# Kernel tuning notes

Measured on AMD Instinct MI355X. Metric: run time of the kernel, lower is better.

## Reference

```python
import jax, jax.numpy as jnp
import numpy as np

EPS = 1e-12  # torch F.normalize eps
NEG = -9999.0  # masked_fill value from the source


def _l2norm(x):
    n = jnp.linalg.norm(x, axis=-1, keepdims=True)
    return x / jnp.maximum(n, EPS)


def _maxsim(q, d, mask_f, mask_b):
    # q: [B,Lq,D]; d: [N,B,Ld,D]; mask: [N,B,Ld]
    rep = _l2norm(d * mask_f[..., None])
    s = jnp.einsum('bqd,nbkd->nbqk', q, rep)  # [N,B,Lq,Ld]
    s = jnp.where(mask_b[:, :, None, :], s, NEG)
    return s.max(axis=-1).sum(axis=-1)  # [N,B]


def setup_inputs() -> dict:
    key = jax.random.key(0)
    k0, k1, k2, k3, k4 = jax.random.split(key, 5)
    B, N, Lq, Ld, D = 128, 8, 32, 256, 128
    return {
        'q_reps': jax.random.normal(k0, (B, Lq, D), jnp.float32),
        'd_cq': jax.random.normal(k1, (N, B, Ld, D), jnp.float32),
        'd_orig': jax.random.normal(k2, (N, B, Ld, D), jnp.float32),
        'd_mask': jax.random.randint(k3, (N, B, Ld), 0, 2).astype(jnp.int32),
        'labels': jax.random.normal(k4, (B, N), jnp.float32),
    }


def reference(q_reps, d_cq, d_orig, d_mask, labels):
    # teacher='default', loss_type='kldiv' path
    q = _l2norm(q_reps)  # normalize query tokens over D
    mask_f = d_mask.astype(q_reps.dtype)
    mask_b = d_mask.astype(bool)
    scores = _maxsim(q, d_cq, mask_f, mask_b).T        # [B,N] student (cq) MaxSim
    scores_label = _maxsim(q, d_orig, mask_f, mask_b).T  # [B,N] teacher (orig) MaxSim
    # softmax->log in the source == log_softmax (same math, stable form)
    log_s = jax.nn.log_softmax(scores, axis=-1)
    log_t = jax.nn.log_softmax(scores_label, axis=-1)
    # KLDivLoss(reduction='batchmean', log_target=True)
    B = scores.shape[0]
    loss = jnp.sum(jnp.exp(log_t) * (log_t - log_s)) / B
    return loss
```

## Files before the change

kernel.cpp:

```cpp
#include <hip/hip_runtime.h>
#include <math.h>

#define Bq 128
#define Nn 8
#define LQ 32
#define LD 256
#define DD 128
#define EPSN 1e-12f
#define NEGV (-9999.0f)

typedef __attribute__((ext_vector_type(8))) short short8v;
typedef __attribute__((ext_vector_type(4))) int   int4v;
typedef __attribute__((ext_vector_type(4))) float f32x4;

__device__ __forceinline__ unsigned bf16_rne_hibits(float x) {
    unsigned u = __float_as_uint(x);
    return (u + 0x7FFFu + ((u >> 16) & 1u)) & 0xFFFF0000u;
}

__global__ __launch_bounds__(256) void qnorm_k(const float* __restrict__ q,
                                               unsigned short* __restrict__ qh,
                                               unsigned short* __restrict__ ql) {
    int row  = blockIdx.x * 4 + (threadIdx.x >> 6);
    int lane = threadIdx.x & 63;
    size_t base = (size_t)row * DD + lane * 2;
    float2 v = *reinterpret_cast<const float2*>(q + base);
    float ss = v.x * v.x + v.y * v.y;
#pragma unroll
    for (int o = 32; o; o >>= 1) ss += __shfl_xor(ss, o);
    float inv = 1.0f / fmaxf(sqrtf(ss), EPSN);
    float x0 = v.x * inv, x1 = v.y * inv;
    unsigned h0 = bf16_rne_hibits(x0), h1 = bf16_rne_hibits(x1);
    float l0 = x0 - __uint_as_float(h0);
    float l1 = x1 - __uint_as_float(h1);
    unsigned g0 = bf16_rne_hibits(l0), g1 = bf16_rne_hibits(l1);
    *reinterpret_cast<unsigned*>(qh + base) = (h0 >> 16) | h1;
    *reinterpret_cast<unsigned*>(ql + base) = (g0 >> 16) | g1;
}

__global__ __launch_bounds__(256) void maxsim_k(const float* __restrict__ d_cq,
                                                const float* __restrict__ d_orig,
                                                const int* __restrict__ mask,
                                                const unsigned short* __restrict__ qh,
                                                const unsigned short* __restrict__ ql,
                                                float* __restrict__ scores) {
    __shared__ float wma[4][32];
    __shared__ float wmb[4][32];

    int nb = blockIdx.x;
    int b  = nb & 127;
    int n  = nb >> 7;

    int tid  = threadIdx.x;
    int w    = tid >> 6;
    int lane = tid & 63;
    int r    = lane & 15;
    int g    = lane >> 4;

    const unsigned short* qh_r = qh + ((size_t)b * LQ + r) * DD + g * 8;
    const unsigned short* ql_r = ql + ((size_t)b * LQ + r) * DD + g * 8;

    f32x4 rm0a = {NEGV, NEGV, NEGV, NEGV}, rm1a = {NEGV, NEGV, NEGV, NEGV};
    f32x4 rm0b = {NEGV, NEGV, NEGV, NEGV}, rm1b = {NEGV, NEGV, NEGV, NEGV};

#define SB __builtin_amdgcn_sched_barrier(0)

#define CVT2(DH, DL, W, X0, X1, SSQ)                                           \
    { unsigned h0 = bf16_rne_hibits(X0), h1 = bf16_rne_hibits(X1);             \
      float lf0 = (X0) - __uint_as_float(h0);                                  \
      float lf1 = (X1) - __uint_as_float(h1);                                  \
      DH[W] = (int)((h0 >> 16) | h1);                                          \
      DL[W] = (int)((bf16_rne_hibits(lf0) >> 16) | bf16_rne_hibits(lf1));      \
      SSQ += (X0)*(X0) + (X1)*(X1); }

#define KSTEP(CA0, CA1, CB0, CB1, KS, PFOFF)                                   \
    {                                                                          \
        short8v a0h = *reinterpret_cast<const short8v*>(qh_r + (KS) * 32);     \
        short8v a0l = *reinterpret_cast<const short8v*>(ql_r + (KS) * 32);     \
        short8v a1h = *reinterpret_cast<const short8v*>(qh_r + 16 * DD + (KS) * 32); \
        short8v a1l = *reinterpret_cast<const short8v*>(ql_r + 16 * DD + (KS) * 32); \
        int4v dhwa, dlwa, dhwb, dlwb;                                          \
        CVT2(dhwa, dlwa, 0, CA0.x, CA0.y, ssqa)                                \
        CVT2(dhwa, dlwa, 1, CA0.z, CA0.w, ssqa)                                \
        CVT2(dhwa, dlwa, 2, CA1.x, CA1.y, ssqa)                                \
        CVT2(dhwa, dlwa, 3, CA1.z, CA1.w, ssqa)                                \
        CA0 = *reinterpret_cast<const float4*>(prow_a + (PFOFF));              \
        CA1 = *reinterpret_cast<const float4*>(prow_a + (PFOFF) + 4);          \
        CVT2(dhwb, dlwb, 0, CB0.x, CB0.y, ssqb)                                \
        CVT2(dhwb, dlwb, 1, CB0.z, CB0.w, ssqb)                                \
        CVT2(dhwb, dlwb, 2, CB1.x, CB1.y, ssqb)                                \
        CVT2(dhwb, dlwb, 3, CB1.z, CB1.w, ssqb)                                \
        CB0 = *reinterpret_cast<const float4*>(prow_b + (PFOFF));              \
        CB1 = *reinterpret_cast<const float4*>(prow_b + (PFOFF) + 4);          \
        short8v dha = __builtin_bit_cast(short8v, dhwa);                       \
        short8v dla = __builtin_bit_cast(short8v, dlwa);                       \
        c0a = __builtin_amdgcn_mfma_f32_16x16x32_bf16(a0h, dha, c0a, 0, 0, 0); \
        c1a = __builtin_amdgcn_mfma_f32_16x16x32_bf16(a1h, dha, c1a, 0, 0, 0); \
        c0a = __builtin_amdgcn_mfma_f32_16x16x32_bf16(a0h, dla, c0a, 0, 0, 0); \
        c1a = __builtin_amdgcn_mfma_f32_16x16x32_bf16(a1h, dla, c1a, 0, 0, 0); \
        c0a = __builtin_amdgcn_mfma_f32_16x16x32_bf16(a0l, dha, c0a, 0, 0, 0); \
        c1a = __builtin_amdgcn_mfma_f32_16x16x32_bf16(a1l, dha, c1a, 0, 0, 0); \
        short8v dhb = __builtin_bit_cast(short8v, dhwb);                       \
        short8v dlb = __builtin_bit_cast(short8v, dlwb);                       \
        c0b = __builtin_amdgcn_mfma_f32_16x16x32_bf16(a0h, dhb, c0b, 0, 0, 0); \
        c1b = __builtin_amdgcn_mfma_f32_16x16x32_bf16(a1h, dhb, c1b, 0, 0, 0); \
        c0b = __builtin_amdgcn_mfma_f32_16x16x32_bf16(a0h, dlb, c0b, 0, 0, 0); \
        c1b = __builtin_amdgcn_mfma_f32_16x16x32_bf16(a1h, dlb, c1b, 0, 0, 0); \
        c0b = __builtin_amdgcn_mfma_f32_16x16x32_bf16(a0l, dhb, c0b, 0, 0, 0); \
        c1b = __builtin_amdgcn_mfma_f32_16x16x32_bf16(a1l, dhb, c1b, 0, 0, 0); \
    }

    const float* prow_a = d_cq   + (size_t)nb * (LD * DD) + (size_t)(w * 64 + r) * DD + g * 8;
    const float* prow_b = d_orig + (size_t)nb * (LD * DD) + (size_t)(w * 64 + r) * DD + g * 8;

    float4 Xa0 = *reinterpret_cast<const float4*>(prow_a);
    float4 Xa1 = *reinterpret_cast<const float4*>(prow_a + 4);
    float4 Xb0 = *reinterpret_cast<const float4*>(prow_b);
    float4 Xb1 = *reinterpret_cast<const float4*>(prow_b + 4);
    float4 Ya0 = *reinterpret_cast<const float4*>(prow_a + 32);
    float4 Ya1 = *reinterpret_cast<const float4*>(prow_a + 36);
    float4 Yb0 = *reinterpret_cast<const float4*>(prow_b + 32);
    float4 Yb1 = *reinterpret_cast<const float4*>(prow_b + 36);

#pragma unroll 1
    for (int nt = 0; nt < 4; ++nt) {
        int drow = w * 64 + nt * 16 + r;

        f32x4 c0a = {0.f, 0.f, 0.f, 0.f}, c1a = {0.f, 0.f, 0.f, 0.f};
        f32x4 c0b = {0.f, 0.f, 0.f, 0.f}, c1b = {0.f, 0.f, 0.f, 0.f};
        float ssqa = 0.0f, ssqb = 0.0f;

        int mk = mask[(size_t)nb * LD + drow];
        int nnoff = (nt < 3) ? 2048 : 0;

        KSTEP(Xa0, Xa1, Xb0, Xb1, 0, 64);         SB;
        KSTEP(Ya0, Ya1, Yb0, Yb1, 1, 96);         SB;
        KSTEP(Xa0, Xa1, Xb0, Xb1, 2, nnoff);      SB;
        KSTEP(Ya0, Ya1, Yb0, Yb1, 3, nnoff + 32); SB;

        ssqa += __shfl_xor(ssqa, 16);  ssqa += __shfl_xor(ssqa, 32);
        ssqb += __shfl_xor(ssqb, 16);  ssqb += __shfl_xor(ssqb, 32);
        float inva = 1.0f / fmaxf(sqrtf(ssqa), EPSN);
        float invb = 1.0f / fmaxf(sqrtf(ssqb), EPSN);

#pragma unroll
        for (int i = 0; i < 4; ++i) {
            rm0a[i] = fmaxf(rm0a[i], mk ? c0a[i] * inva : NEGV);
            rm1a[i] = fmaxf(rm1a[i], mk ? c1a[i] * inva : NEGV);
            rm0b[i] = fmaxf(rm0b[i], mk ? c0b[i] * invb : NEGV);
            rm1b[i] = fmaxf(rm1b[i], mk ? c1b[i] * invb : NEGV);
        }
        prow_a += 16 * DD;
        prow_b += 16 * DD;
    }
#undef KSTEP
#undef CVT2

#pragma unroll
    for (int i = 0; i < 4; ++i) {
#pragma unroll
        for (int o = 1; o <= 8; o <<= 1) {
            rm0a[i] = fmaxf(rm0a[i], __shfl_xor(rm0a[i], o));
            rm1a[i] = fmaxf(rm1a[i], __shfl_xor(rm1a[i], o));
            rm0b[i] = fmaxf(rm0b[i], __shfl_xor(rm0b[i], o));
            rm1b[i] = fmaxf(rm1b[i], __shfl_xor(rm1b[i], o));
        }
    }
    if (r == 0) {
#pragma unroll
        for (int i = 0; i < 4; ++i) {
            wma[w][g * 4 + i]      = rm0a[i];
            wma[w][16 + g * 4 + i] = rm1a[i];
            wmb[w][g * 4 + i]      = rm0b[i];
            wmb[w][16 + g * 4 + i] = rm1b[i];
        }
    }
    __syncthreads();

    if (tid < 64) {
        int tau = tid >> 5, l = tid & 31;
        const float (*wm)[32] = tau ? wmb : wma;
        float v = fmaxf(fmaxf(wm[0][l], wm[1][l]),
                        fmaxf(wm[2][l], wm[3][l]));
#pragma unroll
        for (int o = 1; o <= 16; o <<= 1) v += __shfl_xor(v, o);
        if (l == 0)
            scores[tau * (Bq * Nn) + b * Nn + n] = v;
    }
}

__global__ void loss_k(const float* __restrict__ scores, float* __restrict__ out) {
    int tid = threadIdx.x;
    const float* s = scores + tid * Nn;
    const float* t = scores + Bq * Nn + tid * Nn;
    float sv[Nn], tv[Nn];
#pragma unroll
    for (int n = 0; n < Nn; ++n) { sv[n] = s[n]; tv[n] = t[n]; }
    float ms = sv[0], mt = tv[0];
#pragma unroll
    for (int n = 1; n < Nn; ++n) { ms = fmaxf(ms, sv[n]); mt = fmaxf(mt, tv[n]); }
    float es = 0.0f, et = 0.0f;
#pragma unroll
    for (int n = 0; n < Nn; ++n) { es += expf(sv[n] - ms); et += expf(tv[n] - mt); }
    float lses = ms + logf(es);
    float lset = mt + logf(et);
    double kl = 0.0;
#pragma unroll
    for (int n = 0; n < Nn; ++n) {
        float lt = tv[n] - lset;
        float ls = sv[n] - lses;
        kl += (double)expf(lt) * ((double)lt - (double)ls);
    }
#pragma unroll
    for (int o = 32; o; o >>= 1) kl += __shfl_xor(kl, o);
    __shared__ double part[2];
    if ((tid & 63) == 0) part[tid >> 6] = kl;
    __syncthreads();
    if (tid == 0) out[0] = (float)((part[0] + part[1]) / (double)Bq);
}

extern "C" void kernel_launch(void* const* d_in, const int* in_sizes, int n_in,
                              void* d_out, int out_size, void* d_ws, size_t ws_size,
                              hipStream_t stream) {
    const float* q     = (const float*)d_in[0];
    const float* dcq   = (const float*)d_in[1];
    const float* dorig = (const float*)d_in[2];
    const int*   mask  = (const int*)d_in[3];

    unsigned short* qh = (unsigned short*)d_ws;
    unsigned short* ql = qh + (size_t)Bq * LQ * DD;
    float* scores      = (float*)(ql + (size_t)Bq * LQ * DD);

    qnorm_k<<<(Bq * LQ) / 4, 256, 0, stream>>>(q, qh, ql);
    maxsim_k<<<Nn * Bq, 256, 0, stream>>>(dcq, dorig, mask, qh, ql, scores);
    loss_k<<<1, 128, 0, stream>>>(scores, (float*)d_out);
}
```

Measured before the change: 65.56 us.

## Stage query bf16 split in swizzled LDS and truncate doc split

The query hi/lo bf16 tiles for each batch row are copied once into shared memory, using an XOR swizzle applied at write time in the normalization kernel, and the MFMA A operands are then read from LDS instead of global memory. This removes repeated global/L2 loads of the same query data per k-step and aims to avoid LDS bank conflicts. Separately, the document fp32-to-bf16 hi/lo split now truncates instead of rounding to nearest even, which saves ALU work per element. Truncation slightly changes the split error, although hi+lo still approximates the value closely.

```diff
diff --git a/kernel.cpp b/kernel.cpp
--- a/kernel.cpp
+++ b/kernel.cpp
@@ -34,8 +34,9 @@
     float l0 = x0 - __uint_as_float(h0);
     float l1 = x1 - __uint_as_float(h1);
     unsigned g0 = bf16_rne_hibits(l0), g1 = bf16_rne_hibits(l1);
-    *reinterpret_cast<unsigned*>(qh + base) = (h0 >> 16) | h1;
-    *reinterpret_cast<unsigned*>(ql + base) = (g0 >> 16) | g1;
+    unsigned swz = ((unsigned)(lane * 2)) ^ (((unsigned)row & 7u) << 3);
+    *reinterpret_cast<unsigned*>(qh + (size_t)row * DD + swz) = (h0 >> 16) | h1;
+    *reinterpret_cast<unsigned*>(ql + (size_t)row * DD + swz) = (g0 >> 16) | g1;
 }
 
 __global__ __launch_bounds__(256) void maxsim_k(const float* __restrict__ d_cq,
@@ -44,6 +45,7 @@
                                                 const unsigned short* __restrict__ qh,
                                                 const unsigned short* __restrict__ ql,
                                                 float* __restrict__ scores) {
+    __shared__ float4 qstage[1024];
     __shared__ float wma[4][32];
     __shared__ float wmb[4][32];
 
@@ -57,8 +59,19 @@
     int r    = lane & 15;
     int g    = lane >> 4;
 
-    const unsigned short* qh_r = qh + ((size_t)b * LQ + r) * DD + g * 8;
-    const unsigned short* ql_r = ql + ((size_t)b * LQ + r) * DD + g * 8;
+    {
+        const float4* srch = reinterpret_cast<const float4*>(qh + (size_t)b * LQ * DD);
+        const float4* srcl = reinterpret_cast<const float4*>(ql + (size_t)b * LQ * DD);
+        qstage[tid]       = srch[tid];
+        qstage[tid + 256] = srch[tid + 256];
+        qstage[tid + 512] = srcl[tid];
+        qstage[tid + 768] = srcl[tid + 256];
+    }
+    __syncthreads();
+
+    const unsigned short* qh_lds = reinterpret_cast<const unsigned short*>(qstage);
+    const unsigned short* ql_lds = qh_lds + LQ * DD;
+    unsigned swz8 = ((unsigned)r & 7u) << 3;
 
     f32x4 rm0a = {NEGV, NEGV, NEGV, NEGV}, rm1a = {NEGV, NEGV, NEGV, NEGV};
     f32x4 rm0b = {NEGV, NEGV, NEGV, NEGV}, rm1b = {NEGV, NEGV, NEGV, NEGV};
@@ -66,19 +79,21 @@
 #define SB __builtin_amdgcn_sched_barrier(0)
 
 #define CVT2(DH, DL, W, X0, X1, SSQ)                                           \
-    { unsigned h0 = bf16_rne_hibits(X0), h1 = bf16_rne_hibits(X1);             \
-      float lf0 = (X0) - __uint_as_float(h0);                                  \
-      float lf1 = (X1) - __uint_as_float(h1);                                  \
-      DH[W] = (int)((h0 >> 16) | h1);                                          \
-      DL[W] = (int)((bf16_rne_hibits(lf0) >> 16) | bf16_rne_hibits(lf1));      \
+    { unsigned u0 = __float_as_uint(X0), u1 = __float_as_uint(X1);             \
+      DH[W] = (int)((u0 >> 16) | (u1 & 0xFFFF0000u));                          \
+      float l0 = (X0) - __uint_as_float(u0 & 0xFFFF0000u);                     \
+      float l1 = (X1) - __uint_as_float(u1 & 0xFFFF0000u);                     \
+      DL[W] = (int)((__float_as_uint(l0) >> 16) |                              \
+                    (__float_as_uint(l1) & 0xFFFF0000u));                      \
       SSQ += (X0)*(X0) + (X1)*(X1); }
 
 #define KSTEP(CA0, CA1, CB0, CB1, KS, PFOFF)                                   \
     {                                                                          \
-        short8v a0h = *reinterpret_cast<const short8v*>(qh_r + (KS) * 32);     \
-        short8v a0l = *reinterpret_cast<const short8v*>(ql_r + (KS) * 32);     \
-        short8v a1h = *reinterpret_cast<const short8v*>(qh_r + 16 * DD + (KS) * 32); \
-        short8v a1l = *reinterpret_cast<const short8v*>(ql_r + 16 * DD + (KS) * 32); \
+        unsigned aoff = (((unsigned)(KS) * 32u) + (unsigned)g * 8u) ^ swz8;    \
+        short8v a0h = *reinterpret_cast<const short8v*>(qh_lds + r * DD + aoff);          \
+        short8v a0l = *reinterpret_cast<const short8v*>(ql_lds + r * DD + aoff);          \
+        short8v a1h = *reinterpret_cast<const short8v*>(qh_lds + (r + 16) * DD + aoff);   \
+        short8v a1l = *reinterpret_cast<const short8v*>(ql_lds + (r + 16) * DD + aoff);   \
         int4v dhwa, dlwa, dhwb, dlwb;                                          \
         CVT2(dhwa, dlwa, 0, CA0.x, CA0.y, ssqa)                                \
         CVT2(dhwa, dlwa, 1, CA0.z, CA0.w, ssqa)                                \
```

Result: faster. 63.46 us (-3.2%).
